# Performance work log

Measured on AMD Instinct MI355X. Metric: run time of the kernel, lower is better.

The kernel has to match this reference:

```python
import jax, jax.numpy as jnp
import numpy as np

NUM_BANDS = 31
POOL_SIZES = (4, 8, 16)
GN_GROUPS = 32
GN_EPS = 1e-5


def _interp_matrix(out_size, in_size):
    # PyTorch bilinear, align_corners=False, as a sparse-ish [out, in] matrix
    i = np.arange(out_size)
    src = (i + 0.5) * (in_size / out_size) - 0.5
    src = np.clip(src, 0.0, in_size - 1)
    lo = np.floor(src).astype(np.int64)
    hi = np.minimum(lo + 1, in_size - 1)
    w = src - lo
    M = np.zeros((out_size, in_size), dtype=np.float32)
    np.add.at(M, (i, lo), 1.0 - w)
    np.add.at(M, (i, hi), w)
    return jnp.asarray(M)


def _scale_branch(x, s, conv_w, spectral_w):
    # x: [B, C, H, W]; adaptive avg pool to (s, s) == uniform pooling (H, W % s == 0)
    B, C, H, W = x.shape
    xp = x.reshape(B, C, s, H // s, s, W // s).mean(axis=(3, 5))  # [B, C, s, s]
    qkv = jnp.einsum('bchw,oc->bohw', xp, conv_w)  # 1x1 conv, no bias
    rd = conv_w.shape[0] // 3
    q, k, v = qkv[:, :rd], qkv[:, rd:2 * rd], qkv[:, 2 * rd:]
    g = rd // NUM_BANDS  # bands_per_group
    S = s * s
    q = q.reshape(B, g, NUM_BANDS, S).transpose(0, 3, 1, 2)  # [B, S, g, n]
    k = k.reshape(B, g, NUM_BANDS, S).transpose(0, 3, 2, 1)  # [B, S, n, g]
    v = v.reshape(B, g, NUM_BANDS, S).transpose(0, 3, 1, 2)  # [B, S, g, n]
    scale = g ** (-0.5)
    attn = jnp.einsum('bsgn,nm,bsmh->bsgh', q, spectral_w, k) * scale  # [B, S, g, g]
    attn = jax.nn.softmax(attn, axis=-1)
    out = jnp.einsum('bsgh,bshn->bsgn', attn, v)  # [B, S, g, n]
    out = out.transpose(0, 2, 3, 1).reshape(B, rd, s, s)
    Mh = _interp_matrix(H, s)
    Mw = _interp_matrix(W, s)
    return jnp.einsum('bcij,hi,wj->bchw', out, Mh, Mw)  # bilinear upsample to [B, rd, H, W]


def _group_norm(x, weight, bias):
    B, C, H, W = x.shape
    xg = x.reshape(B, GN_GROUPS, C // GN_GROUPS, H, W)
    mean = xg.mean(axis=(2, 3, 4), keepdims=True)
    var = ((xg - mean) ** 2).mean(axis=(2, 3, 4), keepdims=True)
    xn = ((xg - mean) * jax.lax.rsqrt(var + GN_EPS)).reshape(B, C, H, W)
    return xn * weight[None, :, None, None] + bias[None, :, None, None]


def setup_inputs() -> dict:
    key = jax.random.key(0)
    ks = jax.random.split(key, 12)
    B, C, H, W = 4, 256, 256, 256
    rd = 93  # reduced_dim for dim=256, reduction=4, num_bands=31
    x = jax.random.normal(ks[0], (B, C, H, W), dtype=jnp.float32)
    conv_ws = [jax.random.normal(ks[1 + i], (3 * rd, C), dtype=jnp.float32) * (C ** -0.5) for i in range(3)]
    sws = [jnp.eye(NUM_BANDS, dtype=jnp.float32) * 0.1
           + 0.01 * jax.random.normal(ks[4 + i], (NUM_BANDS, NUM_BANDS), dtype=jnp.float32) for i in range(3)]
    fusion_w = jax.random.normal(ks[7], (C, 3 * rd), dtype=jnp.float32) * ((3 * rd) ** -0.5)
    fusion_b = jax.random.normal(ks[8], (C,), dtype=jnp.float32) * 0.01
    gn_w = jnp.ones((C,), dtype=jnp.float32) + 0.01 * jax.random.normal(ks[9], (C,), dtype=jnp.float32)
    gn_b = 0.01 * jax.random.normal(ks[10], (C,), dtype=jnp.float32)
    return {'x': x, 'conv_w0': conv_ws[0], 'conv_w1': conv_ws[1], 'conv_w2': conv_ws[2],
            'sw0': sws[0], 'sw1': sws[1], 'sw2': sws[2],
            'fusion_w': fusion_w, 'fusion_b': fusion_b, 'gn_w': gn_w, 'gn_b': gn_b}


def reference(x, conv_w0, conv_w1, conv_w2, sw0, sw1, sw2, fusion_w, fusion_b, gn_w, gn_b):
    conv_ws = (conv_w0, conv_w1, conv_w2)
    sws = (sw0, sw1, sw2)
    scale_outputs = [_scale_branch(x, s, cw, sw) for s, cw, sw in zip(POOL_SIZES, conv_ws, sws)]
    fused = jnp.concatenate(scale_outputs, axis=1)  # [B, 3*rd, H, W]
    out = jnp.einsum('bchw,oc->bohw', fused, fusion_w) + fusion_b[None, :, None, None]
    return _group_norm(out + x, gn_w, gn_b)
```

## Files before the change

### kernel.cpp

```cpp
#include <hip/hip_runtime.h>
#include <hip/hip_bf16.h>
#include <math.h>

#define B 4
#define C 256
#define H 256
#define Wd 256

__global__ __launch_bounds__(256) void xreadproj_kernel(
    const float* __restrict__ x,
    float* __restrict__ pool16, float* __restrict__ xp16o,
    float* __restrict__ xp8o, float* __restrict__ xp4o,
    float* __restrict__ sx) {

    __shared__ float P0[16][72];
    __shared__ float SS16[16][68];
    __shared__ float SS8[16][72];
    __shared__ float SS4[16][80];
    __shared__ float Rs[16 * 29];
    __shared__ float rs[4][2];

    int bc = blockIdx.x;
    int t = threadIdx.x;
    int wg = t >> 6, l = t & 63;

    const float4* xp = (const float4*)(x + (size_t)bc * (H * Wd));

    for (int e = t; e < 576; e += 256) {
        int r = e / 36, g = e - r * 36;
        if (g < 8)       P0[r][64 + g] = 0.f;
        else if (g < 10) SS16[r][g - 8] = 0.f;
        else if (g < 12) SS16[r][56 + g] = 0.f;
        else if (g < 16) SS8[r][g - 12] = 0.f;
        else if (g < 20) SS8[r][52 + g] = 0.f;
        else if (g < 28) SS4[r][g - 20] = 0.f;
        else             SS4[r][44 + g] = 0.f;
    }

    float a16, b16, a8, b8, a4, b4;
    {
        float w0 = 4.f * (float)l + 0.5f;
        float s16v = w0 * 0.0625f - 0.5f;
        if (l <= 1 || l >= 62) { a16 = 0.f; b16 = 0.f; }
        else { a16 = s16v - floorf(s16v); b16 = 0.0625f; }
        float s8v = w0 * 0.03125f - 0.5f;
        if (l <= 3 || l >= 60) { a8 = 0.f; b8 = 0.f; }
        else { a8 = s8v - floorf(s8v); b8 = 0.03125f; }
        float s4v = w0 * 0.015625f - 0.5f;
        if (l <= 7 || l >= 56) { a4 = 0.f; b4 = 0.f; }
        else { a4 = s4v - floorf(s4v); b4 = 0.015625f; }
    }

    const int i16 = t >> 4, j16 = t & 15;
    const int i8 = t >> 3, j8 = t & 7;
    const int i4 = (t - 64) >> 2, j4 = (t - 64) & 3;

    float accA = 0.f;
    float accB = 0.f;
    float sx1 = 0.f, sx2 = 0.f;

    float4 v[4], vn[4];
#pragma unroll
    for (int it = 0; it < 4; ++it)
        v[it] = xp[(wg * 4 + it) * 64 + l];

#pragma unroll 1
    for (int k = 0; k < 16; ++k) {
        if (k > 0) {
            int kk = k - 1;
            if (kk >= i16 - 1 && kk <= i16 + 1) {
#pragma unroll
                for (int rl = 0; rl < 16; ++rl) {
                    float src = ((float)(kk * 16 + rl) + 0.5f) * 0.0625f - 0.5f;
                    src = fminf(fmaxf(src, 0.f), 15.f);
                    int lo = (int)src; float fr = src - (float)lo;
                    float w = (i16 == lo) ? (1.f - fr) : ((i16 == lo + 1) ? fr : 0.f);
                    accA += w * Rs[rl * 29 + j16];
                }
            }
            if (t < 64) {
                if (kk >= 2 * i8 - 1 && kk <= 2 * i8 + 2) {
#pragma unroll
                    for (int rl = 0; rl < 16; ++rl) {
                        float src = ((float)(kk * 16 + rl) + 0.5f) * 0.03125f - 0.5f;
                        src = fminf(fmaxf(src, 0.f), 7.f);
                        int lo = (int)src; float fr = src - (float)lo;
                        float w = (i8 == lo) ? (1.f - fr) : ((i8 == lo + 1) ? fr : 0.f);
                        accB += w * Rs[rl * 29 + 16 + j8];
                    }
                }
            } else if (t < 80) {
                if (kk >= 4 * i4 - 2 && kk <= 4 * i4 + 5) {
#pragma unroll
                    for (int rl = 0; rl < 16; ++rl) {
                        float src = ((float)(kk * 16 + rl) + 0.5f) * 0.015625f - 0.5f;
                        src = fminf(fmaxf(src, 0.f), 3.f);
                        int lo = (int)src; float fr = src - (float)lo;
                        float w = (i4 == lo) ? (1.f - fr) : ((i4 == lo + 1) ? fr : 0.f);
                        accB += w * Rs[rl * 29 + 24 + j4];
                    }
                }
            }
        }

#pragma unroll
        for (int it = 0; it < 4; ++it) {
            int r = wg * 4 + it;
            float4 vv = v[it];
            float p0 = (vv.x + vv.y) + (vv.z + vv.w);
            float pw = fmaf(3.f, vv.w, fmaf(2.f, vv.z, vv.y));
            sx1 += p0;
            sx2 += vv.x * vv.x + vv.y * vv.y + vv.z * vv.z + vv.w * vv.w;
            P0[r][l]       = p0;
            SS16[r][2 + l] = fmaf(b16, pw, a16 * p0);
            SS8[r][4 + l]  = fmaf(b8,  pw, a8  * p0);
            SS4[r][8 + l]  = fmaf(b4,  pw, a4  * p0);
        }
        __syncthreads();

        if (k < 15) {
#pragma unroll
            for (int it = 0; it < 4; ++it)
                vn[it] = xp[((k + 1) * 16 + wg * 4 + it) * 64 + l];
        }

        for (int tk = t; tk < 464; tk += 256) {
            if (tk < 256) {
                int r = tk >> 4, j = tk & 15;
                float sum = 0.f;
#pragma unroll
                for (int q = 0; q < 4; ++q)
                    sum += P0[r][4 * j + 2 + q] - SS16[r][4 * j + 4 + q];
#pragma unroll
                for (int q = 0; q < 4; ++q) sum += SS16[r][4 * j + q];
                if (j == 0) sum += (P0[r][0] - SS16[r][2]) + (P0[r][1] - SS16[r][3]);
                Rs[r * 29 + j] = sum;
            } else if (tk < 384) {
                int q2 = tk - 256; int r = q2 >> 3, j = q2 & 7;
                float sum = 0.f;
#pragma unroll
                for (int q = 0; q < 8; ++q)
                    sum += P0[r][8 * j + 4 + q] - SS8[r][8 * j + 8 + q];
#pragma unroll
                for (int q = 0; q < 8; ++q) sum += SS8[r][8 * j + q];
                if (j == 0) {
#pragma unroll
                    for (int q = 0; q < 4; ++q) sum += P0[r][q] - SS8[r][4 + q];
                }
                Rs[r * 29 + 16 + j] = sum;
            } else if (tk < 448) {
                int q2 = tk - 384; int r = q2 >> 2, j = q2 & 3;
                float sum = 0.f;
#pragma unroll
                for (int q = 0; q < 16; ++q)
                    sum += P0[r][16 * j + 8 + q] - SS4[r][16 * j + 16 + q];
#pragma unroll
                for (int q = 0; q < 16; ++q) sum += SS4[r][16 * j + q];
                if (j == 0) {
#pragma unroll
                    for (int q = 0; q < 8; ++q) sum += P0[r][q] - SS4[r][8 + q];
                }
                Rs[r * 29 + 24 + j] = sum;
            } else {
                int j = tk - 448;
                float sum = 0.f;
#pragma unroll
                for (int r2 = 0; r2 < 16; ++r2) {
#pragma unroll
                    for (int q = 0; q < 4; ++q) sum += P0[r2][4 * j + q];
                }
                pool16[(size_t)bc * 256 + k * 16 + j] = sum * (1.f / 256.f);
            }
        }
        __syncthreads();
#pragma unroll
        for (int it = 0; it < 4; ++it) v[it] = vn[it];
    }

    {
        int kk = 15;
        if (kk >= i16 - 1 && kk <= i16 + 1) {
#pragma unroll
            for (int rl = 0; rl < 16; ++rl) {
                float src = ((float)(kk * 16 + rl) + 0.5f) * 0.0625f - 0.5f;
                src = fminf(fmaxf(src, 0.f), 15.f);
                int lo = (int)src; float fr = src - (float)lo;
                float w = (i16 == lo) ? (1.f - fr) : ((i16 == lo + 1) ? fr : 0.f);
                accA += w * Rs[rl * 29 + j16];
            }
        }
        if (t < 64) {
            if (kk >= 2 * i8 - 1 && kk <= 2 * i8 + 2) {
#pragma unroll
                for (int rl = 0; rl < 16; ++rl) {
                    float src = ((float)(kk * 16 + rl) + 0.5f) * 0.03125f - 0.5f;
                    src = fminf(fmaxf(src, 0.f), 7.f);
                    int lo = (int)src; float fr = src - (float)lo;
                    float w = (i8 == lo) ? (1.f - fr) : ((i8 == lo + 1) ? fr : 0.f);
                    accB += w * Rs[rl * 29 + 16 + j8];
                }
            }
        } else if (t < 80) {
            if (kk >= 4 * i4 - 2 && kk <= 4 * i4 + 5) {
#pragma unroll
                for (int rl = 0; rl < 16; ++rl) {
                    float src = ((float)(kk * 16 + rl) + 0.5f) * 0.015625f - 0.5f;
                    src = fminf(fmaxf(src, 0.f), 3.f);
                    int lo = (int)src; float fr = src - (float)lo;
                    float w = (i4 == lo) ? (1.f - fr) : ((i4 == lo + 1) ? fr : 0.f);
                    accB += w * Rs[rl * 29 + 24 + j4];
                }
            }
        }
    }

    xp16o[(size_t)bc * 256 + t] = accA;
    if (t < 64) xp8o[(size_t)bc * 64 + t] = accB;
    else if (t < 80) xp4o[(size_t)bc * 16 + (t - 64)] = accB;

#pragma unroll
    for (int off = 1; off < 64; off <<= 1) {
        sx1 += __shfl_xor(sx1, off);
        sx2 += __shfl_xor(sx2, off);
    }
    if (l == 0) { rs[wg][0] = sx1; rs[wg][1] = sx2; }
    __syncthreads();
    if (t == 0) {
        sx[bc * 2]     = rs[0][0] + rs[1][0] + rs[2][0] + rs[3][0];
        sx[bc * 2 + 1] = rs[0][1] + rs[1][1] + rs[2][1] + rs[3][1];
    }
}

__global__ __launch_bounds__(256) void site_kernel(
    const float* __restrict__ pool16,
    const float* __restrict__ cw0, const float* __restrict__ cw1,
    const float* __restrict__ cw2,
    const float* __restrict__ sw0, const float* __restrict__ sw1,
    const float* __restrict__ sw2,
    const float* __restrict__ fusion_w,
    float* __restrict__ y4, float* __restrict__ y8, float* __restrict__ y16) {

    __shared__ float P[256];
    __shared__ float Wm[961];
    __shared__ float QKV[279];
    __shared__ float QW[93];
    __shared__ float A[9];
    __shared__ float OUTV[93];

    int t = threadIdx.x;
    int blk = blockIdx.x;
    int b = blk / 336;
    int r = blk % 336;

    int s, site, foff;
    const float* cw; const float* sw; float* yout;
    if (r < 256)      { s = 16; site = r;       cw = cw2; sw = sw2; foff = 186; yout = y16; }
    else if (r < 320) { s = 8;  site = r - 256; cw = cw1; sw = sw1; foff = 93;  yout = y8;  }
    else              { s = 4;  site = r - 320; cw = cw0; sw = sw0; foff = 0;   yout = y4;  }
    int i = site / s, j = site % s;

    for (int idx = t; idx < 961; idx += 256) Wm[idx] = sw[idx];

    {
        int f = 16 / s;
        float acc = 0.f;
        int base = (b * 256 + t) * 256;
        for (int ii = 0; ii < f; ++ii)
            for (int jj = 0; jj < f; ++jj)
                acc += pool16[base + (i * f + ii) * 16 + (j * f + jj)];
        P[t] = acc / (float)(f * f);
    }
    __syncthreads();

    for (int o = t; o < 279; o += 256) {
        const float4* wrow = (const float4*)(cw + o * 256);
        float acc = 0.f;
#pragma unroll 8
        for (int c4 = 0; c4 < 64; ++c4) {
            float4 wv = wrow[c4];
            acc += wv.x * P[c4 * 4] + wv.y * P[c4 * 4 + 1] +
                   wv.z * P[c4 * 4 + 2] + wv.w * P[c4 * 4 + 3];
        }
        QKV[o] = acc;
    }
    __syncthreads();

    if (t < 93) {
        int g = t / 31, m = t % 31;
        float acc = 0.f;
        for (int n = 0; n < 31; ++n) acc += QKV[g * 31 + n] * Wm[n * 31 + m];
        QW[t] = acc;
    }
    __syncthreads();
    if (t < 9) {
        int g = t / 3, h = t % 3;
        float acc = 0.f;
        for (int m = 0; m < 31; ++m) acc += QW[g * 31 + m] * QKV[93 + h * 31 + m];
        A[t] = acc * 0.57735026918962576f;
    }
    __syncthreads();
    if (t < 3) {
        float a0 = A[t * 3], a1 = A[t * 3 + 1], a2 = A[t * 3 + 2];
        float mx = fmaxf(a0, fmaxf(a1, a2));
        float e0 = expf(a0 - mx), e1 = expf(a1 - mx), e2 = expf(a2 - mx);
        float inv = 1.0f / (e0 + e1 + e2);
        A[t * 3] = e0 * inv; A[t * 3 + 1] = e1 * inv; A[t * 3 + 2] = e2 * inv;
    }
    __syncthreads();
    if (t < 93) {
        int g = t / 31, n = t % 31;
        OUTV[t] = A[g * 3] * QKV[186 + n] + A[g * 3 + 1] * QKV[186 + 31 + n] +
                  A[g * 3 + 2] * QKV[186 + 62 + n];
    }
    __syncthreads();
    {
        const float* fr = fusion_w + t * 279 + foff;
        float acc = 0.f;
#pragma unroll 31
        for (int c = 0; c < 93; ++c) acc += fr[c] * OUTV[c];
        yout[(size_t)(b * 256 + t) * (s * s) + site] = acc;
    }
}

__global__ __launch_bounds__(256) void chanstat_kernel(
    const float* __restrict__ y4, const float* __restrict__ y8,
    const float* __restrict__ y16,
    const float* __restrict__ xp4, const float* __restrict__ xp8,
    const float* __restrict__ xp16,
    const float* __restrict__ sx, const float* __restrict__ fusion_b,
    double* __restrict__ chanS) {

    __shared__ float G1616[256], G168[128], G164[64], G88[64], G84[32], G44[16];
    __shared__ float cs[28];
    __shared__ float ybuf[336], xbuf[336];
    __shared__ float Tm[256];
    __shared__ float red[8];

    int t = threadIdx.x;
    int bc = blockIdx.x;

    for (int e = t; e < 588; e += 256) {
        if (e >= 560) {
            int q = e - 560; int sC, iC;
            if (q < 16) { sC = 16; iC = q; }
            else if (q < 24) { sC = 8; iC = q - 16; }
            else { sC = 4; iC = q - 24; }
            int R = 256 / sC;
            int lo = max(0, R * iC - R / 2), hi = min(256, R * iC + (3 * R) / 2);
            float Rinv = 1.f / (float)R, smax = (float)(sC - 1);
            float a = 0.f;
            for (int h = lo; h < hi; ++h) {
                float src = fminf(fmaxf(((float)h + 0.5f) * Rinv - 0.5f, 0.f), smax);
                int lq = (int)src; float fr = src - (float)lq;
                a += (iC == lq) ? (1.f - fr) : ((iC == lq + 1) ? fr : 0.f);
            }
            cs[q] = a;
            continue;
        }
        int sA, sB, iA, iB; float* dst; int off;
        if (e < 256)      { sA = 16; sB = 16; iA = e >> 4; iB = e & 15; dst = G1616; off = e; }
        else if (e < 384) { int q = e - 256; sA = 16; sB = 8; iA = q >> 3; iB = q & 7; dst = G168; off = q; }
        else if (e < 448) { int q = e - 384; sA = 16; sB = 4; iA = q >> 2; iB = q & 3; dst = G164; off = q; }
        else if (e < 512) { int q = e - 448; sA = 8;  sB = 8; iA = q >> 3; iB = q & 7; dst = G88;  off = q; }
        else if (e < 544) { int q = e - 512; sA = 8;  sB = 4; iA = q >> 2; iB = q & 3; dst = G84;  off = q; }
        else              { int q = e - 544; sA = 4;  sB = 4; iA = q >> 2; iB = q & 3; dst = G44;  off = q; }
        int RA = 256 / sA, RB = 256 / sB;
        int lo = max(max(0, RA * iA - RA / 2), RB * iB - RB / 2);
        int hi = min(min(256, RA * iA + (3 * RA) / 2), RB * iB + (3 * RB) / 2);
        float RAi = 1.f / (float)RA, RBi = 1.f / (float)RB;
        float smA = (float)(sA - 1), smB = (float)(sB - 1);
        float a = 0.f;
        for (int h = lo; h < hi; ++h) {
            float sa = fminf(fmaxf(((float)h + 0.5f) * RAi - 0.5f, 0.f), smA);
            int la = (int)sa; float fa = sa - (float)la;
            float wa = (iA == la) ? (1.f - fa) : ((iA == la + 1) ? fa : 0.f);
            float sb = fminf(fmaxf(((float)h + 0.5f) * RBi - 0.5f, 0.f), smB);
            int lb = (int)sb; float fb_ = sb - (float)lb;
            float wb = (iB == lb) ? (1.f - fb_) : ((iB == lb + 1) ? fb_ : 0.f);
            a += wa * wb;
        }
        dst[off] = a;
    }

    size_t bcs = (size_t)bc;
    ybuf[t] = y16[bcs * 256 + t];
    xbuf[t] = xp16[bcs * 256 + t];
    if (t < 64) { ybuf[256 + t] = y8[bcs * 64 + t]; xbuf[256 + t] = xp8[bcs * 64 + t]; }
    else if (t < 80) { ybuf[256 + t] = y4[bcs * 16 + (t - 64)]; xbuf[256 + t] = xp4[bcs * 16 + (t - 64)]; }
    __syncthreads();

    float pu = 0.f, pv = 0.f;
    for (int e = t; e < 336; e += 256) {
        float yv = ybuf[e];
        pv += 2.f * yv * xbuf[e];
        int ci, cj;
        if (e < 256)      { ci = e >> 4;               cj = e & 15; }
        else if (e < 320) { ci = 16 + ((e - 256) >> 3); cj = 16 + ((e - 256) & 7); }
        else              { ci = 24 + ((e - 320) >> 2); cj = 24 + ((e - 320) & 3); }
        pu += yv * cs[ci] * cs[cj];
    }

    for (int p = 0; p < 6; ++p) {
        const float* Gp; int sA, sB, yAoff, yBoff; float factor;
        switch (p) {
            case 0: Gp = G1616; sA = 16; sB = 16; yAoff = 0;   yBoff = 0;   factor = 1.f; break;
            case 1: Gp = G168;  sA = 16; sB = 8;  yAoff = 0;   yBoff = 256; factor = 2.f; break;
            case 2: Gp = G164;  sA = 16; sB = 4;  yAoff = 0;   yBoff = 320; factor = 2.f; break;
            case 3: Gp = G88;   sA = 8;  sB = 8;  yAoff = 256; yBoff = 256; factor = 1.f; break;
            case 4: Gp = G84;   sA = 8;  sB = 4;  yAoff = 256; yBoff = 320; factor = 2.f; break;
            default:Gp = G44;   sA = 4;  sB = 4;  yAoff = 320; yBoff = 320; factor = 1.f; break;
        }
        __syncthreads();
        int nT = sB * sA;
        if (t < nT) {
            int iB = t / sA, jA = t - iB * sA;
            float a = 0.f;
            for (int jB = 0; jB < sB; ++jB)
                a += Gp[jA * sB + jB] * ybuf[yBoff + iB * sB + jB];
            Tm[t] = a;
        }
        __syncthreads();
        int nB = sA * sA;
        if (t < nB) {
            int iA = t / sA, jA = t - iA * sA;
            float a = 0.f;
            for (int iB = 0; iB < sB; ++iB)
                a += Gp[iA * sB + iB] * Tm[iB * sA + jA];
            pv += factor * ybuf[yAoff + t] * a;
        }
    }

#pragma unroll
    for (int off = 1; off < 64; off <<= 1) {
        pu += __shfl_xor(pu, off);
        pv += __shfl_xor(pv, off);
    }
    __syncthreads();
    if ((t & 63) == 0) { red[(t >> 6) * 2] = pu; red[(t >> 6) * 2 + 1] = pv; }
    __syncthreads();
    if (t == 0) {
        float puT = red[0] + red[2] + red[4] + red[6];
        float pvT = red[1] + red[3] + red[5] + red[7];
        float fb = fusion_b[bc & 255];
        float s1 = sx[bc * 2], s2 = sx[bc * 2 + 1];
        double S1 = (double)s1 + 65536.0 * (double)fb + (double)puT;
        double S2 = (double)s2 + 2.0 * (double)fb * (double)s1 +
                    65536.0 * (double)fb * (double)fb +
                    2.0 * (double)fb * (double)puT + (double)pvT;
        chanS[bc * 2] = S1;
        chanS[bc * 2 + 1] = S2;
    }
}

__global__ __launch_bounds__(128) void gnfold_kernel(
    const double* __restrict__ chanS, float* __restrict__ stats_g) {
    int t = threadIdx.x;
    int b = t >> 5, g = t & 31;
    double gS1 = 0.0, gS2 = 0.0;
    for (int c8 = 0; c8 < 8; ++c8) {
        int c = g * 8 + c8;
        gS1 += chanS[(b * 256 + c) * 2];
        gS2 += chanS[(b * 256 + c) * 2 + 1];
    }
    double mean = gS1 / 524288.0;
    double var  = gS2 / 524288.0 - mean * mean;
    stats_g[t * 2] = (float)mean;
    stats_g[t * 2 + 1] = (float)(1.0 / sqrt(var + 1e-5));
}

__global__ __launch_bounds__(256) void write_kernel(
    const float* __restrict__ x,
    const float* __restrict__ ws_y4, const float* __restrict__ ws_y8,
    const float* __restrict__ ws_y16,
    const float* __restrict__ fusion_b,
    const float* __restrict__ gn_w, const float* __restrict__ gn_b,
    const float* __restrict__ stats_g,
    float* __restrict__ out) {

    __shared__ float ly16[256], ly8[64], ly4[16];
    __shared__ float2 rbd16[16][16];
    __shared__ float2 rbd8[16][8];
    __shared__ float2 rbd4[16][4];

    int blk = (B * C * 16 - 1) - blockIdx.x;
    int hblk = blk & 15;
    int c = (blk >> 4) & 255;
    int b = blk >> 12;
    int t = threadIdx.x;

    ly16[t] = ws_y16[(size_t)(b * 256 + c) * 256 + t];
    if (t < 64) ly8[t] = ws_y8[(size_t)(b * 256 + c) * 64 + t];
    if (t < 16) ly4[t] = ws_y4[(size_t)(b * 256 + c) * 16 + t];
    __syncthreads();

    for (int idx = t; idx < 448; idx += 256) {
        int r = idx / 28;
        int q = idx - r * 28;
        int h = hblk * 16 + r;
        if (q < 16) {
            float src = (h + 0.5f) * 0.0625f - 0.5f;
            src = fminf(fmaxf(src, 0.f), 15.f);
            int lo = (int)src; float wf = src - lo; int hi = min(lo + 1, 15);
            float rb = (1.f - wf) * ly16[lo * 16 + q] + wf * ly16[hi * 16 + q];
            rbd16[r][q].x = rb;
            if (q > 0) rbd16[r][q - 1].y = rb;
            if (q == 15) rbd16[r][15].y = rb;
        } else if (q < 24) {
            int jj = q - 16;
            float src = (h + 0.5f) * 0.03125f - 0.5f;
            src = fminf(fmaxf(src, 0.f), 7.f);
            int lo = (int)src; float wf = src - lo; int hi = min(lo + 1, 7);
            float rb = (1.f - wf) * ly8[lo * 8 + jj] + wf * ly8[hi * 8 + jj];
            rbd8[r][jj].x = rb;
            if (jj > 0) rbd8[r][jj - 1].y = rb;
            if (jj == 7) rbd8[r][7].y = rb;
        } else {
            int jj = q - 24;
            float src = (h + 0.5f) * 0.015625f - 0.5f;
            src = fminf(fmaxf(src, 0.f), 3.f);
            int lo = (int)src; float wf = src - lo; int hi = min(lo + 1, 3);
            float rb = (1.f - wf) * ly4[lo * 4 + jj] + wf * ly4[hi * 4 + jj];
            rbd4[r][jj].x = rb;
            if (jj > 0) rbd4[r][jj - 1].y = rb;
            if (jj == 3) rbd4[r][3].y = rb;
        }
    }
    __syncthreads();

    int w4 = t & 63;
    int wg = t >> 6;
    int w0 = w4 * 4;

    int jlo16[4], jlo8[4], jlo4[4];
    float ww16[4], ww8[4], ww4[4];
#pragma unroll
    for (int p = 0; p < 4; ++p) {
        int w = w0 + p;
        float s16 = fminf(fmaxf((w + 0.5f) * 0.0625f - 0.5f, 0.f), 15.f);
        jlo16[p] = (int)s16; ww16[p] = s16 - jlo16[p];
        float s8 = fminf(fmaxf((w + 0.5f) * 0.03125f - 0.5f, 0.f), 7.f);
        jlo8[p] = (int)s8; ww8[p] = s8 - jlo8[p];
        float s4 = fminf(fmaxf((w + 0.5f) * 0.015625f - 0.5f, 0.f), 3.f);
        jlo4[p] = (int)s4; ww4[p] = s4 - jlo4[p];
    }

    float fb_c = fusion_b[c];
    int gidx = c >> 3;
    float mean = stats_g[(b * 32 + gidx) * 2];
    float rstd = stats_g[(b * 32 + gidx) * 2 + 1];
    float gwc = gn_w[c], gbc = gn_b[c];

    const float4* xp = (const float4*)(x + (size_t)(b * 256 + c) * (H * Wd));
    float4* op = (float4*)(out + (size_t)(b * 256 + c) * (H * Wd));

#pragma unroll
    for (int it = 0; it < 4; ++it) {
        int r = it * 4 + wg;
        int idx4 = (hblk * 16 + r) * 64 + w4;
        float4 xv = xp[idx4];
        float res[4];
        float px[4] = {xv.x, xv.y, xv.z, xv.w};
#pragma unroll
        for (int p = 0; p < 4; ++p) {
            float f = fb_c;
            float2 v16 = rbd16[r][jlo16[p]];
            f += (1.f - ww16[p]) * v16.x + ww16[p] * v16.y;
            float2 v8 = rbd8[r][jlo8[p]];
            f += (1.f - ww8[p]) * v8.x + ww8[p] * v8.y;
            float2 v4 = rbd4[r][jlo4[p]];
            f += (1.f - ww4[p]) * v4.x + ww4[p] * v4.y;
            float tv = px[p] + f;
            res[p] = (tv - mean) * rstd * gwc + gbc;
        }
        op[idx4] = make_float4(res[0], res[1], res[2], res[3]);
    }
}

extern "C" void kernel_launch(void* const* d_in, const int* in_sizes, int n_in,
                              void* d_out, int out_size, void* d_ws, size_t ws_size,
                              hipStream_t stream) {
    const float* x   = (const float*)d_in[0];
    const float* cw0 = (const float*)d_in[1];
    const float* cw1 = (const float*)d_in[2];
    const float* cw2 = (const float*)d_in[3];
    const float* sw0 = (const float*)d_in[4];
    const float* sw1 = (const float*)d_in[5];
    const float* sw2 = (const float*)d_in[6];
    const float* fw  = (const float*)d_in[7];
    const float* fb  = (const float*)d_in[8];
    const float* gw  = (const float*)d_in[9];
    const float* gb  = (const float*)d_in[10];
    float* out = (float*)d_out;

    float* ws     = (float*)d_ws;
    float* pool16 = ws;
    float* y4     = pool16 + 262144;
    float* y8     = y4 + 16384;
    float* y16    = y8 + 65536;
    float* xp16   = y16 + 262144;
    float* xp8    = xp16 + 262144;
    float* xp4    = xp8 + 65536;
    float* sx     = xp4 + 16384;
    float* statsg = sx + 2048;
    double* chanS = (double*)(statsg + 256);

    xreadproj_kernel<<<B * C, 256, 0, stream>>>(x, pool16, xp16, xp8, xp4, sx);
    site_kernel<<<B * 336, 256, 0, stream>>>(pool16, cw0, cw1, cw2,
                                             sw0, sw1, sw2, fw, y4, y8, y16);
    chanstat_kernel<<<B * C, 256, 0, stream>>>(y4, y8, y16, xp4, xp8, xp16,
                                               sx, fb, chanS);
    gnfold_kernel<<<1, 128, 0, stream>>>(chanS, statsg);
    write_kernel<<<B * C * 16, 256, 0, stream>>>(x, y4, y8, y16, fb, gw, gb,
                                                 statsg, out);
}
```

Before: 254.4 us.

## Precompute bilinear Gram once in xreadproj and fold GN stats into write kernel

The bilinear-interpolation Gram coefficients were recomputed serially by every chanstat block. They are now computed once, in parallel across 588 blocks of the x-reading kernel using 64-lane reductions, and the result is loaded from global memory. The single-block gnfold kernel is removed and each write block derives its group mean and rstd from chanS. This drops one launch and redundant work, at the cost of 16384 write blocks each doing a small double-precision fold plus one extra shared read.

```diff
diff --git a/kernel.cpp b/kernel.cpp
--- a/kernel.cpp
+++ b/kernel.cpp
@@ -11,7 +11,7 @@
     const float* __restrict__ x,
     float* __restrict__ pool16, float* __restrict__ xp16o,
     float* __restrict__ xp8o, float* __restrict__ xp4o,
-    float* __restrict__ sx) {
+    float* __restrict__ sx, float* __restrict__ gram) {
 
     __shared__ float P0[16][72];
     __shared__ float SS16[16][68];
@@ -229,6 +229,50 @@
         sx[bc * 2]     = rs[0][0] + rs[1][0] + rs[2][0] + rs[3][0];
         sx[bc * 2 + 1] = rs[0][1] + rs[1][1] + rs[2][1] + rs[3][1];
     }
+
+    if (bc < 588 && t < 64) {
+        int e = bc;
+        float acc = 0.f;
+        if (e >= 560) {
+            int q = e - 560; int sC, iC;
+            if (q < 16) { sC = 16; iC = q; }
+            else if (q < 24) { sC = 8; iC = q - 16; }
+            else { sC = 4; iC = q - 24; }
+            int R = 256 / sC;
+            int lo = max(0, R * iC - R / 2), hi = min(256, R * iC + (3 * R) / 2);
+            float Rinv = 1.f / (float)R, smax = (float)(sC - 1);
+            for (int h = lo + t; h < hi; h += 64) {
+                float src = fminf(fmaxf(((float)h + 0.5f) * Rinv - 0.5f, 0.f), smax);
+                int lq = (int)src; float fr = src - (float)lq;
+                acc += (iC == lq) ? (1.f - fr) : ((iC == lq + 1) ? fr : 0.f);
+            }
+        } else {
+            int sA, sB, iA, iB;
+            if (e < 256)      { sA = 16; sB = 16; iA = e >> 4; iB = e & 15; }
+            else if (e < 384) { int q = e - 256; sA = 16; sB = 8; iA = q >> 3; iB = q & 7; }
+            else if (e < 448) { int q = e - 384; sA = 16; sB = 4; iA = q >> 2; iB = q & 3; }
+            else if (e < 512) { int q = e - 448; sA = 8;  sB = 8; iA = q >> 3; iB = q & 7; }
+            else if (e < 544) { int q = e - 512; sA = 8;  sB = 4; iA = q >> 2; iB = q & 3; }
+            else              { int q = e - 544; sA = 4;  sB = 4; iA = q >> 2; iB = q & 3; }
+            int RA = 256 / sA, RB = 256 / sB;
+            int lo = max(max(0, RA * iA - RA / 2), RB * iB - RB / 2);
+            int hi = min(min(256, RA * iA + (3 * RA) / 2), RB * iB + (3 * RB) / 2);
+            float RAi = 1.f / (float)RA, RBi = 1.f / (float)RB;
+            float smA = (float)(sA - 1), smB = (float)(sB - 1);
+            for (int h = lo + t; h < hi; h += 64) {
+                float sa = fminf(fmaxf(((float)h + 0.5f) * RAi - 0.5f, 0.f), smA);
+                int la = (int)sa; float fa = sa - (float)la;
+                float wa = (iA == la) ? (1.f - fa) : ((iA == la + 1) ? fa : 0.f);
+                float sb = fminf(fmaxf(((float)h + 0.5f) * RBi - 0.5f, 0.f), smB);
+                int lb = (int)sb; float fb_ = sb - (float)lb;
+                float wb = (iB == lb) ? (1.f - fb_) : ((iB == lb + 1) ? fb_ : 0.f);
+                acc += wa * wb;
+            }
+        }
+#pragma unroll
+        for (int off = 1; off < 64; off <<= 1) acc += __shfl_xor(acc, off);
+        if (t == 0) gram[e] = acc;
+    }
 }
 
 __global__ __launch_bounds__(256) void site_kernel(
@@ -328,10 +372,10 @@
     const float* __restrict__ xp4, const float* __restrict__ xp8,
     const float* __restrict__ xp16,
     const float* __restrict__ sx, const float* __restrict__ fusion_b,
+    const float* __restrict__ gram,
     double* __restrict__ chanS) {
 
-    __shared__ float G1616[256], G168[128], G164[64], G88[64], G84[32], G44[16];
-    __shared__ float cs[28];
+    __shared__ float Gs[588];
     __shared__ float ybuf[336], xbuf[336];
     __shared__ float Tm[256];
     __shared__ float red[8];
@@ -339,48 +383,15 @@
     int t = threadIdx.x;
     int bc = blockIdx.x;
 
-    for (int e = t; e < 588; e += 256) {
-        if (e >= 560) {
-            int q = e - 560; int sC, iC;
-            if (q < 16) { sC = 16; iC = q; }
-            else if (q < 24) { sC = 8; iC = q - 16; }
-            else { sC = 4; iC = q - 24; }
-            int R = 256 / sC;
-            int lo = max(0, R * iC - R / 2), hi = min(256, R * iC + (3 * R) / 2);
-            float Rinv = 1.f / (float)R, smax = (float)(sC - 1);
-            float a = 0.f;
-            for (int h = lo; h < hi; ++h) {
-                float src = fminf(fmaxf(((float)h + 0.5f) * Rinv - 0.5f, 0.f), smax);
-                int lq = (int)src; float fr = src - (float)lq;
-                a += (iC == lq) ? (1.f - fr) : ((iC == lq + 1) ? fr : 0.f);
-            }
-            cs[q] = a;
-            continue;
-        }
-        int sA, sB, iA, iB; float* dst; int off;
-        if (e < 256)      { sA = 16; sB = 16; iA = e >> 4; iB = e & 15; dst = G1616; off = e; }
-        else if (e < 384) { int q = e - 256; sA = 16; sB = 8; iA = q >> 3; iB = q & 7; dst = G168; off = q; }
-        else if (e < 448) { int q = e - 384; sA = 16; sB = 4; iA = q >> 2; iB = q & 3; dst = G164; off = q; }
-        else if (e < 512) { int q = e - 448; sA = 8;  sB = 8; iA = q >> 3; iB = q & 7; dst = G88;  off = q; }
-        else if (e < 544) { int q = e - 512; sA = 8;  sB = 4; iA = q >> 2; iB = q & 3; dst = G84;  off = q; }
-        else              { int q = e - 544; sA = 4;  sB = 4; iA = q >> 2; iB = q & 3; dst = G44;  off = q; }
-        int RA = 256 / sA, RB = 256 / sB;
-        int lo = max(max(0, RA * iA - RA / 2), RB * iB - RB / 2);
-        int hi = min(min(256, RA * iA + (3 * RA) / 2), RB * iB + (3 * RB) / 2);
-        float RAi = 1.f / (float)RA, RBi = 1.f / (float)RB;
-        float smA = (float)(sA - 1), smB = (float)(sB - 1);
-        float a = 0.f;
-        for (int h = lo; h < hi; ++h) {
-            float sa = fminf(fmaxf(((float)h + 0.5f) * RAi - 0.5f, 0.f), smA);
-            int la = (int)sa; float fa = sa - (float)la;
-            float wa = (iA == la) ? (1.f - fa) : ((iA == la + 1) ? fa : 0.f);
-            float sb = fminf(fmaxf(((float)h + 0.5f) * RBi - 0.5f, 0.f), smB);
-            int lb = (int)sb; float fb_ = sb - (float)lb;
-            float wb = (iB == lb) ? (1.f - fb_) : ((iB == lb + 1) ? fb_ : 0.f);
-            a += wa * wb;
-        }
-        dst[off] = a;
-    }
+    for (int e = t; e < 588; e += 256) Gs[e] = gram[e];
+
+    const float* G1616 = Gs;
+    const float* G168  = Gs + 256;
+    const float* G164  = Gs + 384;
+    const float* G88   = Gs + 448;
+    const float* G84   = Gs + 512;
+    const float* G44   = Gs + 544;
+    const float* cs    = Gs + 560;
 
     size_t bcs = (size_t)bc;
     ybuf[t] = y16[bcs * 256 + t];
@@ -452,41 +463,41 @@
     }
 }
 
-__global__ __launch_bounds__(128) void gnfold_kernel(
-    const double* __restrict__ chanS, float* __restrict__ stats_g) {
-    int t = threadIdx.x;
-    int b = t >> 5, g = t & 31;
-    double gS1 = 0.0, gS2 = 0.0;
-    for (int c8 = 0; c8 < 8; ++c8) {
-        int c = g * 8 + c8;
-        gS1 += chanS[(b * 256 + c) * 2];
-        gS2 += chanS[(b * 256 + c) * 2 + 1];
-    }
-    double mean = gS1 / 524288.0;
-    double var  = gS2 / 524288.0 - mean * mean;
-    stats_g[t * 2] = (float)mean;
-    stats_g[t * 2 + 1] = (float)(1.0 / sqrt(var + 1e-5));
-}
-
 __global__ __launch_bounds__(256) void write_kernel(
     const float* __restrict__ x,
     const float* __restrict__ ws_y4, const float* __restrict__ ws_y8,
     const float* __restrict__ ws_y16,
     const float* __restrict__ fusion_b,
     const float* __restrict__ gn_w, const float* __restrict__ gn_b,
-    const float* __restrict__ stats_g,
+    const double* __restrict__ chanS,
     float* __restrict__ out) {
 
     __shared__ float ly16[256], ly8[64], ly4[16];
     __shared__ float2 rbd16[16][16];
     __shared__ float2 rbd8[16][8];
     __shared__ float2 rbd4[16][4];
+    __shared__ float sstat[2];
 
     int blk = (B * C * 16 - 1) - blockIdx.x;
     int hblk = blk & 15;
     int c = (blk >> 4) & 255;
     int b = blk >> 12;
     int t = threadIdx.x;
+
+    if (t == 0) {
+        int gidx = c >> 3;
+        const double* cS = chanS + ((size_t)(b * 256 + gidx * 8)) * 2;
+        double gS1 = 0.0, gS2 = 0.0;
+#pragma unroll
+        for (int c8 = 0; c8 < 8; ++c8) {
+            gS1 += cS[c8 * 2];
+            gS2 += cS[c8 * 2 + 1];
+        }
+        double meand = gS1 / 524288.0;
+        double vard  = gS2 / 524288.0 - meand * meand;
+        sstat[0] = (float)meand;
+        sstat[1] = (float)(1.0 / sqrt(vard + 1e-5));
+    }
 
     ly16[t] = ws_y16[(size_t)(b * 256 + c) * 256 + t];
     if (t < 64) ly8[t] = ws_y8[(size_t)(b * 256 + c) * 64 + t];
@@ -545,9 +556,8 @@
     }
 
     float fb_c = fusion_b[c];
-    int gidx = c >> 3;
-    float mean = stats_g[(b * 32 + gidx) * 2];
-    float rstd = stats_g[(b * 32 + gidx) * 2 + 1];
+    float mean = sstat[0];
+    float rstd = sstat[1];
     float gwc = gn_w[c], gbc = gn_b[c];
 
     const float4* xp = (const float4*)(x + (size_t)(b * 256 + c) * (H * Wd));
@@ -601,15 +611,15 @@
     float* xp8    = xp16 + 262144;
     float* xp4    = xp8 + 65536;
     float* sx     = xp4 + 16384;
-    float* statsg = sx + 2048;
-    double* chanS = (double*)(statsg + 256);
-
-    xreadproj_kernel<<<B * C, 256, 0, stream>>>(x, pool16, xp16, xp8, xp4, sx);
+    float* gramb  = sx + 2048;
+    double* chanS = (double*)(gramb + 640);
+
+    xreadproj_kernel<<<B * C, 256, 0, stream>>>(x, pool16, xp16, xp8, xp4, sx,
+                                                gramb);
     site_kernel<<<B * 336, 256, 0, stream>>>(pool16, cw0, cw1, cw2,
                                              sw0, sw1, sw2, fw, y4, y8, y16);
     chanstat_kernel<<<B * C, 256, 0, stream>>>(y4, y8, y16, xp4, xp8, xp16,
-                                               sx, fb, chanS);
-    gnfold_kernel<<<1, 128, 0, stream>>>(chanS, statsg);
+                                               sx, fb, gramb, chanS);
     write_kernel<<<B * C * 16, 256, 0, stream>>>(x, y4, y8, y16, fb, gw, gb,
-                                                 statsg, out);
+                                                 chanS, out);
 }
```

Measured after the change: 238.0 us. 6.5% less time.
